# Kernel optimization log

Measured on AMD Instinct MI355X. Metric: run time of the kernel, lower is better.

## Reference

```python
import jax, jax.numpy as jnp
import numpy as np

RECON_W = 0.1
CONT_W = 0.2
EPS = 1e-7  # BCE log clamp (torch clamps log at -100; eps-clip is the jax analogue)


def setup_inputs() -> dict:
    key = jax.random.key(0)
    k1, k2, k3, k4 = jax.random.split(key, 4)
    B, M = 256, 4096
    predictions = jax.random.uniform(k1, (B, M, 9), dtype=jnp.float32)
    targets = jax.random.uniform(k2, (B, M, 9), dtype=jnp.float32)
    reconstructed = jax.random.normal(k3, (B, 1, 128, 128), dtype=jnp.float32)
    images = jax.random.normal(k4, (B, 1, 128, 128), dtype=jnp.float32)
    return {"predictions": predictions, "targets": targets,
            "reconstructed": reconstructed, "images": images}


def _continuity_loss(p3, valid_mask):
    # p3: [B, M, 2]; valid_mask: [B, M] bool
    # For each valid slot i, find the next valid slot j > i and accumulate
    # mean(|p3[i] - p3[j]|) -- vectorized replacement for the ragged double loop.
    B, M, _ = p3.shape
    idx = jnp.arange(M, dtype=jnp.int32)
    BIG = jnp.int32(M)
    pos = jnp.where(valid_mask, idx[None, :], BIG)              # [B, M]
    # suffix min over j >= i of pos, then shift to get strict j > i
    suf = jnp.flip(jax.lax.cummin(jnp.flip(pos, axis=1), axis=1), axis=1)
    nxt = jnp.concatenate([suf[:, 1:], jnp.full((B, 1), BIG, jnp.int32)], axis=1)
    pair_valid = valid_mask & (nxt < BIG)                       # [B, M]
    nxt_c = jnp.clip(nxt, 0, M - 1)
    p3_next = jnp.take_along_axis(p3, nxt_c[..., None], axis=1)  # [B, M, 2]
    dist = jnp.abs(p3 - p3_next).mean(axis=-1)                  # [B, M]
    return jnp.sum(dist * pair_valid.astype(p3.dtype)) / B


def _loss(predictions, targets, reconstructed, images):
    target_curves = targets[..., :8]
    target_validity = targets[..., 8:9]
    valid_mask = target_validity[..., 0] > 0.5                  # [B, M]
    fmask = valid_mask.astype(predictions.dtype)
    n_valid = jnp.sum(fmask)

    def masked_l1(pred, tgt, width):
        num = jnp.sum(jnp.abs(pred - tgt) * fmask[..., None])
        return jnp.where(n_valid > 0, num / jnp.maximum(n_valid * width, 1.0), 0.0)

    coord_loss = masked_l1(predictions[..., :6], target_curves[..., :6], 6.0)
    width_loss = masked_l1(predictions[..., 6:8], target_curves[..., 6:8], 2.0)

    p = jnp.clip(predictions[..., 8:9], EPS, 1.0 - EPS)
    t = target_validity
    validity_loss = jnp.mean(-(t * jnp.log(p) + (1.0 - t) * jnp.log(1.0 - p)))

    continuity_loss = _continuity_loss(predictions[..., 4:6], valid_mask)
    reconstruction_loss = jnp.mean((reconstructed - images) ** 2)

    total = (coord_loss + width_loss + 2.0 * validity_loss
             + CONT_W * continuity_loss + RECON_W * reconstruction_loss)
    return total


def reference(predictions, targets, reconstructed, images):
    return _loss(predictions, targets, reconstructed, images)
```

## Files before the change

### kernel.cpp

```cpp
#include <hip/hip_runtime.h>
#include <math.h>

#define B_DIM 256
#define M_DIM 4096
#define EPSV 1e-7f
#define THREADS 1024
#define CHUNK 1024
#define CHUNK_F4 (CHUNK * 9 / 4)
#define NCHUNK (M_DIM / CHUNK)
#define ROW_F4 (M_DIM * 9 / 4)
#define RECON_F4_PER_BLOCK ((B_DIM * 128 * 128 / 4) / B_DIM)


__global__ __launch_bounds__(THREADS, 4) void fused_loss_kernel(
    const float4* __restrict__ pred4, const float4* __restrict__ tgt4,
    const float4* __restrict__ rec4, const float4* __restrict__ img4,
    float* __restrict__ blk_out)
{
    __shared__ float s_pred[CHUNK * 9];
    __shared__ float s_tgt[CHUNK * 9];
    __shared__ float s_p4[M_DIM];
    __shared__ float s_p5[M_DIM];
    __shared__ unsigned long long s_words[M_DIM / 64];
    __shared__ float s_red[16][6];

    const int b    = blockIdx.x;
    const int t    = threadIdx.x;
    const int lane = t & 63;
    const int wave = t >> 6;

    float recon_s = 0.f;
    {
        const float4* rb = rec4 + (size_t)b * RECON_F4_PER_BLOCK;
        const float4* ib = img4 + (size_t)b * RECON_F4_PER_BLOCK;
        #pragma unroll
        for (int i = 0; i < RECON_F4_PER_BLOCK / THREADS; ++i) {
            int idx = i * THREADS + t;
            float4 r = rb[idx]; float4 m = ib[idx];
            float d0 = r.x - m.x, d1 = r.y - m.y, d2 = r.z - m.z, d3 = r.w - m.w;
            recon_s += d0 * d0 + d1 * d1 + d2 * d2 + d3 * d3;
        }
    }

    const float4* pb = pred4 + (size_t)b * ROW_F4;
    const float4* tb = tgt4  + (size_t)b * ROW_F4;

    float coord_s = 0.f, width_s = 0.f, val_s = 0.f, nval_s = 0.f;

    for (int c = 0; c < NCHUNK; ++c) {
        const float4* pc = pb + c * CHUNK_F4;
        const float4* tc = tb + c * CHUNK_F4;

        if (c) __syncthreads();
        #pragma unroll
        for (int i = 0; i < 3; ++i) {
            int idx = i * THREADS + t;
            if (idx < CHUNK_F4) {
                ((float4*)s_pred)[idx] = pc[idx];
                ((float4*)s_tgt)[idx]  = tc[idx];
            }
        }
        __syncthreads();

        const float* pe = s_pred + t * 9;
        const float* te = s_tgt  + t * 9;
        float p0 = pe[0], p1 = pe[1], p2 = pe[2], p3 = pe[3], p4 = pe[4],
              p5 = pe[5], p6 = pe[6], p7 = pe[7], p8 = pe[8];
        float t0 = te[0], t1 = te[1], t2 = te[2], t3 = te[3], t4 = te[4],
              t5 = te[5], t6 = te[6], t7 = te[7], t8 = te[8];

        bool valid = (t8 > 0.5f);
        float fm = valid ? 1.f : 0.f;
        coord_s += fm * (fabsf(p0 - t0) + fabsf(p1 - t1) + fabsf(p2 - t2) +
                         fabsf(p3 - t3) + fabsf(p4 - t4) + fabsf(p5 - t5));
        width_s += fm * (fabsf(p6 - t6) + fabsf(p7 - t7));
        nval_s  += fm;

        float pc8 = fminf(fmaxf(p8, EPSV), 1.0f - EPSV);
        val_s += -(t8 * __logf(pc8) + (1.0f - t8) * __logf(1.0f - pc8));

        const int m = c * CHUNK + t;
        s_p4[m] = p4;
        s_p5[m] = p5;
        unsigned long long bal = __ballot(valid);
        if (lane == 0) s_words[c * 16 + wave] = bal;
    }
    __syncthreads();

    float cont_s = 0.f;
    #pragma unroll
    for (int p = 0; p < 4; ++p) {
        const int m   = p * 1024 + t;
        const int w   = m >> 6;
        const int bit = m & 63;
        unsigned long long wv = s_words[w];
        if ((wv >> bit) & 1ULL) {
            unsigned long long mask = wv & ((bit == 63) ? 0ULL : (~0ULL << (bit + 1)));
            int nxt = -1;
            if (mask) {
                nxt = (w << 6) + __builtin_ctzll(mask);
            } else {
                for (int w2 = w + 1; w2 < (M_DIM / 64); ++w2) {
                    unsigned long long mw = s_words[w2];
                    if (mw) { nxt = (w2 << 6) + __builtin_ctzll(mw); break; }
                }
            }
            if (nxt >= 0) {
                cont_s += 0.5f * (fabsf(s_p4[m] - s_p4[nxt]) +
                                  fabsf(s_p5[m] - s_p5[nxt]));
            }
        }
    }

    float vals[6] = {coord_s, width_s, val_s, nval_s, cont_s, recon_s};
    #pragma unroll
    for (int i = 0; i < 6; ++i) {
        float v = vals[i];
        #pragma unroll
        for (int off = 32; off > 0; off >>= 1) v += __shfl_down(v, off, 64);
        vals[i] = v;
    }
    if (lane == 0) {
        #pragma unroll
        for (int i = 0; i < 6; ++i) s_red[wave][i] = vals[i];
    }
    __syncthreads();
    if (t == 0) {
        float acc[6] = {0.f, 0.f, 0.f, 0.f, 0.f, 0.f};
        for (int wv = 0; wv < 16; ++wv)
            #pragma unroll
            for (int i = 0; i < 6; ++i) acc[i] += s_red[wv][i];
        float* r = blk_out + b * 8;
        #pragma unroll
        for (int i = 0; i < 6; ++i) r[i] = acc[i];
    }
}

__global__ __launch_bounds__(256) void finalize_kernel(
    const float* __restrict__ ws, float* __restrict__ out)
{
    const int t = threadIdx.x;
    const float* rb = ws + t * 8;
    float v[6];
    #pragma unroll
    for (int i = 0; i < 6; ++i) v[i] = rb[i];

    __shared__ float sred[4][6];
    int lane = t & 63, wave = t >> 6;
    #pragma unroll
    for (int i = 0; i < 6; ++i) {
        float x = v[i];
        #pragma unroll
        for (int off = 32; off > 0; off >>= 1) x += __shfl_down(x, off, 64);
        v[i] = x;
    }
    if (lane == 0)
        #pragma unroll
        for (int i = 0; i < 6; ++i) sred[wave][i] = v[i];
    __syncthreads();
    if (t == 0) {
        double a[6];
        #pragma unroll
        for (int i = 0; i < 6; ++i)
            a[i] = (double)sred[0][i] + (double)sred[1][i] +
                   (double)sred[2][i] + (double)sred[3][i];
        double coord_num = a[0], width_num = a[1], val_sum = a[2],
               nv = a[3], cont = a[4], recon = a[5];

        double coord = (nv > 0.0) ? coord_num / fmax(nv * 6.0, 1.0) : 0.0;
        double width = (nv > 0.0) ? width_num / fmax(nv * 2.0, 1.0) : 0.0;
        double validity = val_sum / ((double)B_DIM * (double)M_DIM);
        double contl    = cont / (double)B_DIM;
        double reconl   = recon / ((double)B_DIM * 128.0 * 128.0);

        out[0] = (float)(coord + width + 2.0 * validity +
                         0.2 * contl + 0.1 * reconl);
    }
}

extern "C" void kernel_launch(void* const* d_in, const int* in_sizes, int n_in,
                              void* d_out, int out_size, void* d_ws, size_t ws_size,
                              hipStream_t stream) {
    const float* pred = (const float*)d_in[0];
    const float* tgt  = (const float*)d_in[1];
    const float* rec  = (const float*)d_in[2];
    const float* img  = (const float*)d_in[3];
    float* ws = (float*)d_ws;

    fused_loss_kernel<<<B_DIM, THREADS, 0, stream>>>(
        (const float4*)pred, (const float4*)tgt,
        (const float4*)rec, (const float4*)img, ws);
    finalize_kernel<<<1, 256, 0, stream>>>(ws, (float*)d_out);
}
```

Measured before the change: 135.1 us.

## Register double-buffer prediction/target chunks to overlap global loads with compute

```diff
diff --git a/kernel.cpp b/kernel.cpp
--- a/kernel.cpp
+++ b/kernel.cpp
@@ -10,6 +10,7 @@
 #define NCHUNK (M_DIM / CHUNK)
 #define ROW_F4 (M_DIM * 9 / 4)
 #define RECON_F4_PER_BLOCK ((B_DIM * 128 * 128 / 4) / B_DIM)
+#define TAIL (CHUNK_F4 - 2 * THREADS)
 
 
 __global__ __launch_bounds__(THREADS, 4) void fused_loss_kernel(
@@ -29,6 +30,18 @@
     const int lane = t & 63;
     const int wave = t >> 6;
 
+    const float4* pb = pred4 + (size_t)b * ROW_F4;
+    const float4* tb = tgt4  + (size_t)b * ROW_F4;
+
+    float4 Pa[3], Ta[3], Pb[3], Tb[3];
+
+    {
+        const float4* pc = pb;  const float4* tc = tb;
+        Pa[0] = pc[t];          Ta[0] = tc[t];
+        Pa[1] = pc[t + 1024];   Ta[1] = tc[t + 1024];
+        if (t < TAIL) { Pa[2] = pc[t + 2048]; Ta[2] = tc[t + 2048]; }
+    }
+
     float recon_s = 0.f;
     {
         const float4* rb = rec4 + (size_t)b * RECON_F4_PER_BLOCK;
@@ -42,25 +55,35 @@
         }
     }
 
-    const float4* pb = pred4 + (size_t)b * ROW_F4;
-    const float4* tb = tgt4  + (size_t)b * ROW_F4;
-
     float coord_s = 0.f, width_s = 0.f, val_s = 0.f, nval_s = 0.f;
 
+    #pragma unroll
     for (int c = 0; c < NCHUNK; ++c) {
-        const float4* pc = pb + c * CHUNK_F4;
-        const float4* tc = tb + c * CHUNK_F4;
-
         if (c) __syncthreads();
-        #pragma unroll
-        for (int i = 0; i < 3; ++i) {
-            int idx = i * THREADS + t;
-            if (idx < CHUNK_F4) {
-                ((float4*)s_pred)[idx] = pc[idx];
-                ((float4*)s_tgt)[idx]  = tc[idx];
+
+        {
+            float4* P = (c & 1) ? Pb : Pa;
+            float4* T = (c & 1) ? Tb : Ta;
+            ((float4*)s_pred)[t]        = P[0];
+            ((float4*)s_tgt)[t]         = T[0];
+            ((float4*)s_pred)[t + 1024] = P[1];
+            ((float4*)s_tgt)[t + 1024]  = T[1];
+            if (t < TAIL) {
+                ((float4*)s_pred)[t + 2048] = P[2];
+                ((float4*)s_tgt)[t + 2048]  = T[2];
             }
         }
         __syncthreads();
+
+        if (c < NCHUNK - 1) {
+            const float4* pc = pb + (c + 1) * CHUNK_F4;
+            const float4* tc = tb + (c + 1) * CHUNK_F4;
+            float4* P = (c & 1) ? Pa : Pb;
+            float4* T = (c & 1) ? Ta : Tb;
+            P[0] = pc[t];          T[0] = tc[t];
+            P[1] = pc[t + 1024];   T[1] = tc[t + 1024];
+            if (t < TAIL) { P[2] = pc[t + 2048]; T[2] = tc[t + 2048]; }
+        }
 
         const float* pe = s_pred + t * 9;
         const float* te = s_tgt  + t * 9;
```

Result: slower. 162.0 us (+19.9%).

## Software-pipeline chunk loads through registers to overlap global loads with compute

Applied to the files above, without the earlier changes.

```diff
diff --git a/kernel.cpp b/kernel.cpp
--- a/kernel.cpp
+++ b/kernel.cpp
@@ -10,9 +10,33 @@
 #define NCHUNK (M_DIM / CHUNK)
 #define ROW_F4 (M_DIM * 9 / 4)
 #define RECON_F4_PER_BLOCK ((B_DIM * 128 * 128 / 4) / B_DIM)
-
-
-__global__ __launch_bounds__(THREADS, 4) void fused_loss_kernel(
+#define TAIL (CHUNK_F4 - 2 * THREADS)
+
+
+#define LOADC(cc, P0, P1, P2, T0, T1, T2)                      \
+    do {                                                       \
+        const float4* pc_ = pb + (cc) * CHUNK_F4;              \
+        const float4* tc_ = tb + (cc) * CHUNK_F4;              \
+        P0 = pc_[t];        T0 = tc_[t];                       \
+        P1 = pc_[t + 1024]; T1 = tc_[t + 1024];                \
+        if (t < TAIL) { P2 = pc_[t + 2048]; T2 = tc_[t + 2048]; } \
+    } while (0)
+
+#define STOREC(P0, P1, P2, T0, T1, T2)                         \
+    do {                                                       \
+        ((float4*)s_pred)[t]        = P0;                      \
+        ((float4*)s_tgt)[t]         = T0;                      \
+        ((float4*)s_pred)[t + 1024] = P1;                      \
+        ((float4*)s_tgt)[t + 1024]  = T1;                      \
+        if (t < TAIL) {                                        \
+            ((float4*)s_pred)[t + 2048] = P2;                  \
+            ((float4*)s_tgt)[t + 2048]  = T2;                  \
+        }                                                      \
+    } while (0)
+
+__global__ void __launch_bounds__(THREADS)
+__attribute__((amdgpu_waves_per_eu(4, 4)))
+fused_loss_kernel(
     const float4* __restrict__ pred4, const float4* __restrict__ tgt4,
     const float4* __restrict__ rec4, const float4* __restrict__ img4,
     float* __restrict__ blk_out)
@@ -29,6 +53,41 @@
     const int lane = t & 63;
     const int wave = t >> 6;
 
+    const float4* pb = pred4 + (size_t)b * ROW_F4;
+    const float4* tb = tgt4  + (size_t)b * ROW_F4;
+
+    float coord_s = 0.f, width_s = 0.f, val_s = 0.f, nval_s = 0.f;
+
+    auto consume = [&](int c) {
+        const float* pe = s_pred + t * 9;
+        const float* te = s_tgt  + t * 9;
+        float p0 = pe[0], p1 = pe[1], p2 = pe[2], p3 = pe[3], p4 = pe[4],
+              p5 = pe[5], p6 = pe[6], p7 = pe[7], p8 = pe[8];
+        float t0 = te[0], t1 = te[1], t2 = te[2], t3 = te[3], t4 = te[4],
+              t5 = te[5], t6 = te[6], t7 = te[7], t8 = te[8];
+
+        bool valid = (t8 > 0.5f);
+        float fm = valid ? 1.f : 0.f;
+        coord_s += fm * (fabsf(p0 - t0) + fabsf(p1 - t1) + fabsf(p2 - t2) +
+                         fabsf(p3 - t3) + fabsf(p4 - t4) + fabsf(p5 - t5));
+        width_s += fm * (fabsf(p6 - t6) + fabsf(p7 - t7));
+        nval_s  += fm;
+
+        float pc8 = fminf(fmaxf(p8, EPSV), 1.0f - EPSV);
+        val_s += -(t8 * __logf(pc8) + (1.0f - t8) * __logf(1.0f - pc8));
+
+        const int m = c * CHUNK + t;
+        s_p4[m] = p4;
+        s_p5[m] = p5;
+        unsigned long long bal = __ballot(valid);
+        if (lane == 0) s_words[c * 16 + wave] = bal;
+    };
+
+    float4 PA0, PA1, PA2, TA0, TA1, TA2;
+    float4 PB0, PB1, PB2, TB0, TB1, TB2;
+
+    LOADC(0, PA0, PA1, PA2, TA0, TA1, TA2);
+
     float recon_s = 0.f;
     {
         const float4* rb = rec4 + (size_t)b * RECON_F4_PER_BLOCK;
@@ -42,49 +101,28 @@
         }
     }
 
-    const float4* pb = pred4 + (size_t)b * ROW_F4;
-    const float4* tb = tgt4  + (size_t)b * ROW_F4;
-
-    float coord_s = 0.f, width_s = 0.f, val_s = 0.f, nval_s = 0.f;
-
-    for (int c = 0; c < NCHUNK; ++c) {
-        const float4* pc = pb + c * CHUNK_F4;
-        const float4* tc = tb + c * CHUNK_F4;
-
-        if (c) __syncthreads();
-        #pragma unroll
-        for (int i = 0; i < 3; ++i) {
-            int idx = i * THREADS + t;
-            if (idx < CHUNK_F4) {
-                ((float4*)s_pred)[idx] = pc[idx];
-                ((float4*)s_tgt)[idx]  = tc[idx];
-            }
-        }
-        __syncthreads();
-
-        const float* pe = s_pred + t * 9;
-        const float* te = s_tgt  + t * 9;
-        float p0 = pe[0], p1 = pe[1], p2 = pe[2], p3 = pe[3], p4 = pe[4],
-              p5 = pe[5], p6 = pe[6], p7 = pe[7], p8 = pe[8];
-        float t0 = te[0], t1 = te[1], t2 = te[2], t3 = te[3], t4 = te[4],
-              t5 = te[5], t6 = te[6], t7 = te[7], t8 = te[8];
-
-        bool valid = (t8 > 0.5f);
-        float fm = valid ? 1.f : 0.f;
-        coord_s += fm * (fabsf(p0 - t0) + fabsf(p1 - t1) + fabsf(p2 - t2) +
-                         fabsf(p3 - t3) + fabsf(p4 - t4) + fabsf(p5 - t5));
-        width_s += fm * (fabsf(p6 - t6) + fabsf(p7 - t7));
-        nval_s  += fm;
-
-        float pc8 = fminf(fmaxf(p8, EPSV), 1.0f - EPSV);
-        val_s += -(t8 * __logf(pc8) + (1.0f - t8) * __logf(1.0f - pc8));
-
-        const int m = c * CHUNK + t;
-        s_p4[m] = p4;
-        s_p5[m] = p5;
-        unsigned long long bal = __ballot(valid);
-        if (lane == 0) s_words[c * 16 + wave] = bal;
-    }
+    STOREC(PA0, PA1, PA2, TA0, TA1, TA2);
+    __syncthreads();
+    LOADC(1, PB0, PB1, PB2, TB0, TB1, TB2);
+    consume(0);
+
+    __syncthreads();
+    STOREC(PB0, PB1, PB2, TB0, TB1, TB2);
+    __syncthreads();
+    LOADC(2, PA0, PA1, PA2, TA0, TA1, TA2);
+    consume(1);
+
+    __syncthreads();
+    STOREC(PA0, PA1, PA2, TA0, TA1, TA2);
+    __syncthreads();
+    LOADC(3, PB0, PB1, PB2, TB0, TB1, TB2);
+    consume(2);
+
+    __syncthreads();
+    STOREC(PB0, PB1, PB2, TB0, TB1, TB2);
+    __syncthreads();
+    consume(3);
+
     __syncthreads();
 
     float cont_s = 0.f;
```

Result: faster. 131.9 us (-2.4%).
